# Kernel tuning notes

Measured on AMD Instinct MI355X. Metric: run time of the kernel, lower is better.

Reference implementation:

```python
import jax, jax.numpy as jnp
import numpy as np

B, T, HID = 16, 512, 1024
NH, NKV, D = 8, 4, 128
THETA = 10000.0


def setup_inputs() -> dict:
    key = jax.random.key(0)
    k0, k1, k2, k3, k4 = jax.random.split(key, 5)
    s = 0.02
    return {
        "hidden_states": jax.random.normal(k0, (B, T, HID), dtype=jnp.float32),
        "Wq": s * jax.random.normal(k1, (HID, NH * D), dtype=jnp.float32),
        "Wk": s * jax.random.normal(k2, (HID, NKV * D), dtype=jnp.float32),
        "Wv": s * jax.random.normal(k3, (HID, NKV * D), dtype=jnp.float32),
        "Wo": s * jax.random.normal(k4, (NH * D, HID), dtype=jnp.float32),
    }


def _rotate_half(x):
    x1, x2 = x[..., : x.shape[-1] // 2], x[..., x.shape[-1] // 2:]
    return jnp.concatenate((-x2, x1), axis=-1)


def reference(hidden_states, Wq, Wk, Wv, Wo):
    b, t, _ = hidden_states.shape
    # projections -> [B, H, T, D]
    q = (hidden_states @ Wq).reshape(b, t, NH, D).transpose(0, 2, 1, 3)
    k = (hidden_states @ Wk).reshape(b, t, NKV, D).transpose(0, 2, 1, 3)
    v = (hidden_states @ Wv).reshape(b, t, NKV, D).transpose(0, 2, 1, 3)

    # RoPE: cos/sin [T, D]
    inv_freq = 1.0 / (THETA ** (jnp.arange(0, D, 2, dtype=jnp.float32) / D))
    freqs = jnp.outer(jnp.arange(t, dtype=jnp.float32), inv_freq)
    emb = jnp.concatenate((freqs, freqs), axis=-1)
    cos, sin = jnp.cos(emb), jnp.sin(emb)
    q = q * cos + _rotate_half(q) * sin
    k = k * cos + _rotate_half(k) * sin

    # repeat_interleave KV heads to match query heads (GQA)
    groups = NH // NKV
    k = jnp.repeat(k, groups, axis=1)  # [B, NH, T, D]
    v = jnp.repeat(v, groups, axis=1)

    scale = 1.0 / jnp.sqrt(jnp.float32(D))
    attn = jnp.einsum("bhtd,bhsd->bhts", q, k) * scale  # [B, NH, T, T]
    causal = jnp.triu(jnp.ones((t, t), dtype=bool), k=1)
    attn = jnp.where(causal, -jnp.inf, attn)
    attn = jax.nn.softmax(attn, axis=-1)  # dropout p=0 (eval)

    out = jnp.einsum("bhts,bhsd->bhtd", attn, v)
    out = out.transpose(0, 2, 1, 3).reshape(b, t, NH * D)
    return out @ Wo  # [B, T, HID]
```

## Files before the change

### kernel.cpp

```cpp
#include <hip/hip_runtime.h>
#include <hip/hip_bf16.h>
#include <math.h>

#define Bn 16
#define Tn 512
#define HIDn 1024
#define NHn 8
#define NKVn 4
#define Dn 128

typedef __attribute__((ext_vector_type(8))) short short8;
typedef __attribute__((ext_vector_type(4))) float floatx4;

__device__ __forceinline__ short bf16r(float f) {
  __hip_bfloat16 h = __float2bfloat16(f);
  return *(short*)&h;
}
__device__ __forceinline__ float bf16f(short s) {
  __hip_bfloat16 h = *(__hip_bfloat16*)&s;
  return __bfloat162float(h);
}

__device__ __forceinline__ void g2l16(const short* g, short* l) {
  __builtin_amdgcn_global_load_lds(
      (const __attribute__((address_space(1))) void*)g,
      (__attribute__((address_space(3))) void*)l, 16, 0, 0);
}

__global__ __launch_bounds__(256) void prep_kernel(const float* __restrict__ X,
                                                   const float* __restrict__ Wq,
                                                   const float* __restrict__ Wk,
                                                   const float* __restrict__ Wv,
                                                   const float* __restrict__ Wo,
                                                   short* __restrict__ Xb,
                                                   short* __restrict__ BtQKV,
                                                   short* __restrict__ Wot) {
  __shared__ float tile[32][33];
  int bid = blockIdx.x;
  if (bid < 4096) {
    int i = bid * 256 + threadIdx.x;
    const float4* p = reinterpret_cast<const float4*>(X) + (size_t)i * 2;
    float4 a = p[0], b = p[1];
    short8 o;
    o[0] = bf16r(a.x); o[1] = bf16r(a.y); o[2] = bf16r(a.z); o[3] = bf16r(a.w);
    o[4] = bf16r(b.x); o[5] = bf16r(b.y); o[6] = bf16r(b.z); o[7] = bf16r(b.w);
    reinterpret_cast<short8*>(Xb)[i] = o;
    return;
  }
  int t = bid - 4096;
  const float* in;
  short* out;
  int N;
  if (t < 1024)      { in = Wq; out = BtQKV;               N = 1024; }
  else if (t < 1536) { t -= 1024; in = Wk; out = BtQKV + 1024 * 1024; N = 512; }
  else if (t < 2048) { t -= 1536; in = Wv; out = BtQKV + 1536 * 1024; N = 512; }
  else               { t -= 2048; in = Wo; out = Wot;                N = 1024; }
  int ntx = N >> 5;
  int n0 = (t % ntx) * 32, k0 = (t / ntx) * 32;
  int tx = threadIdx.x & 31, ty = threadIdx.x >> 5;
  for (int i = 0; i < 32; i += 8)
    tile[ty + i][tx] = in[(size_t)(k0 + ty + i) * N + n0 + tx];
  __syncthreads();
  for (int i = 0; i < 32; i += 8)
    out[(size_t)(n0 + ty + i) * 1024 + k0 + tx] = bf16r(tile[tx][ty + i]);
}

__global__ __launch_bounds__(256) void gemm_qkv(const short* __restrict__ A,
                                                const short* __restrict__ Bt,
                                                short* __restrict__ Cqkv,
                                                short* __restrict__ Vt) {
  __shared__ __align__(16) short SH[128 * 136];
  short* As = SH;
  short* Bs = SH + 128 * 64;
  const int K = 1024, N = 2048;
  const int tid = threadIdx.x;
  const int wave = tid >> 6, lane = tid & 63;
  const int quad = lane >> 4, l16 = lane & 15;
  const int wrow = wave >> 1, wcol = wave & 1;
  const int m0 = blockIdx.y * 128, n0 = blockIdx.x * 128;
  floatx4 acc[4][4];
  for (int mi = 0; mi < 4; ++mi)
    for (int ni = 0; ni < 4; ++ni)
      acc[mi][ni] = (floatx4){0.f, 0.f, 0.f, 0.f};

  for (int kt = 0; kt < K; kt += 64) {
#pragma unroll
    for (int v = 0; v < 4; ++v) {
      int s = tid + v * 256;
      int r = s >> 3;
      int c = (s & 7) ^ (r & 7);
      short* dstA = As + (size_t)(v * 256 + wave * 64) * 8;
      g2l16(&A[(size_t)(m0 + r) * K + kt + c * 8], dstA);
      short* dstB = Bs + (size_t)(v * 256 + wave * 64) * 8;
      g2l16(&Bt[(size_t)(n0 + r) * K + kt + c * 8], dstB);
    }
    __syncthreads();
#pragma unroll
    for (int kc = 0; kc < 2; ++kc) {
      short8 af[4], bfr[4];
#pragma unroll
      for (int mi = 0; mi < 4; ++mi) {
        int R = wrow * 64 + mi * 16 + l16;
        int pos = (kc * 4 + quad) ^ (R & 7);
        af[mi] = *(short8*)&As[R * 64 + pos * 8];
      }
#pragma unroll
      for (int ni = 0; ni < 4; ++ni) {
        int R = wcol * 64 + ni * 16 + l16;
        int pos = (kc * 4 + quad) ^ (R & 7);
        bfr[ni] = *(short8*)&Bs[R * 64 + pos * 8];
      }
#pragma unroll
      for (int mi = 0; mi < 4; ++mi)
#pragma unroll
        for (int ni = 0; ni < 4; ++ni)
          acc[mi][ni] = __builtin_amdgcn_mfma_f32_16x16x32_bf16(af[mi], bfr[ni], acc[mi][ni], 0, 0, 0);
    }
    __syncthreads();
  }

  const int bx = blockIdx.x;
  if (bx < 12) {
#pragma unroll
    for (int mi = 0; mi < 4; ++mi)
#pragma unroll
      for (int ni = 0; ni < 4; ++ni)
#pragma unroll
        for (int r = 0; r < 4; ++r) {
          int row = m0 + wrow * 64 + mi * 16 + quad * 4 + r;
          int col = n0 + wcol * 64 + ni * 16 + l16;
          Cqkv[(size_t)row * N + col] = bf16r(acc[mi][ni][r]);
        }
  } else {
#pragma unroll
    for (int mi = 0; mi < 4; ++mi)
#pragma unroll
      for (int ni = 0; ni < 4; ++ni)
#pragma unroll
        for (int r = 0; r < 4; ++r) {
          int tl = wrow * 64 + mi * 16 + quad * 4 + r;
          int dl = wcol * 64 + ni * 16 + l16;
          SH[dl * 136 + tl] = bf16r(acc[mi][ni][r]);
        }
    __syncthreads();
    int kv = bx - 12, b = m0 >> 9, t0 = m0 & (Tn - 1);
#pragma unroll
    for (int k2 = 0; k2 < 8; ++k2) {
      int c = k2 * 256 + tid;
      int d = c >> 4, toff = (c & 15) << 3;
      short8 v = *(short8*)&SH[d * 136 + toff];
      *(short8*)&Vt[((size_t)(b * NKVn + kv) * 128 + d) * Tn + t0 + toff] = v;
    }
  }
}

__global__ void rope_k_kernel(short* __restrict__ C) {
  int idx = blockIdx.x * blockDim.x + threadIdx.x;
  int vec = idx & 7;
  int head = (idx >> 3) & 3;
  int bt = idx >> 5;
  int t = bt & (Tn - 1);
  int i0 = vec * 8;
  size_t base = (size_t)bt * 2048 + 1024 + head * 128 + i0;
  short8 x1 = *(short8*)&C[base];
  short8 x2 = *(short8*)&C[base + 64];
  short8 o1, o2;
  float tf = (float)t;
#pragma unroll
  for (int j = 0; j < 8; ++j) {
    float a = tf * exp2f(-0.2076205059f * (float)(i0 + j));
    float s, c;
    sincosf(a, &s, &c);
    float v1 = bf16f(x1[j]), v2 = bf16f(x2[j]);
    o1[j] = bf16r(v1 * c - v2 * s);
    o2[j] = bf16r(v2 * c + v1 * s);
  }
  *(short8*)&C[base] = o1;
  *(short8*)&C[base + 64] = o2;
}

template <bool OUTF32>
__global__ __launch_bounds__(256) void gemm_bt(const short* __restrict__ A,
                                               const short* __restrict__ Bt,
                                               void* __restrict__ Cout,
                                               int M, int N, int K) {
  __shared__ __align__(16) short As[128 * 64];
  __shared__ __align__(16) short Bs[128 * 64];
  const int tid = threadIdx.x;
  const int wave = tid >> 6, lane = tid & 63;
  const int quad = lane >> 4, l16 = lane & 15;
  const int wrow = wave >> 1, wcol = wave & 1;
  const int m0 = blockIdx.y * 128, n0 = blockIdx.x * 128;
  floatx4 acc[4][4];
  for (int mi = 0; mi < 4; ++mi)
    for (int ni = 0; ni < 4; ++ni)
      acc[mi][ni] = (floatx4){0.f, 0.f, 0.f, 0.f};

  for (int kt = 0; kt < K; kt += 64) {
#pragma unroll
    for (int v = 0; v < 4; ++v) {
      int s = tid + v * 256;
      int r = s >> 3;
      int c = (s & 7) ^ (r & 7);
      short* dstA = (short*)As + (size_t)(v * 256 + wave * 64) * 8;
      g2l16(&A[(size_t)(m0 + r) * K + kt + c * 8], dstA);
      short* dstB = (short*)Bs + (size_t)(v * 256 + wave * 64) * 8;
      g2l16(&Bt[(size_t)(n0 + r) * K + kt + c * 8], dstB);
    }
    __syncthreads();
#pragma unroll
    for (int kc = 0; kc < 2; ++kc) {
      short8 af[4], bfr[4];
#pragma unroll
      for (int mi = 0; mi < 4; ++mi) {
        int R = wrow * 64 + mi * 16 + l16;
        int pos = (kc * 4 + quad) ^ (R & 7);
        af[mi] = *(short8*)&As[R * 64 + pos * 8];
      }
#pragma unroll
      for (int ni = 0; ni < 4; ++ni) {
        int R = wcol * 64 + ni * 16 + l16;
        int pos = (kc * 4 + quad) ^ (R & 7);
        bfr[ni] = *(short8*)&Bs[R * 64 + pos * 8];
      }
#pragma unroll
      for (int mi = 0; mi < 4; ++mi)
#pragma unroll
        for (int ni = 0; ni < 4; ++ni)
          acc[mi][ni] = __builtin_amdgcn_mfma_f32_16x16x32_bf16(af[mi], bfr[ni], acc[mi][ni], 0, 0, 0);
    }
    __syncthreads();
  }
#pragma unroll
  for (int mi = 0; mi < 4; ++mi)
#pragma unroll
    for (int ni = 0; ni < 4; ++ni)
#pragma unroll
      for (int r = 0; r < 4; ++r) {
        int row = m0 + wrow * 64 + mi * 16 + quad * 4 + r;
        int col = n0 + wcol * 64 + ni * 16 + l16;
        if (OUTF32)
          ((float*)Cout)[(size_t)row * N + col] = acc[mi][ni][r];
        else
          ((short*)Cout)[(size_t)row * N + col] = bf16r(acc[mi][ni][r]);
      }
}

__global__ __launch_bounds__(256) void attn_kernel(const short* __restrict__ Cqkv,
                                                   const short* __restrict__ Vt,
                                                   short* __restrict__ Aout) {
  __shared__ __align__(16) short Ks[64 * 128];
  __shared__ __align__(16) short Vs[128 * 64];
  __shared__ short Ps[4][16][72];
  const int tid = threadIdx.x;
  const int wave = tid >> 6, lane = tid & 63;
  const int quad = lane >> 4, l16 = lane & 15;
  const int blk = blockIdx.x;
  const int qt = 7 - (blk >> 7);
  const int h = blk & 7, b = (blk >> 3) & 15;
  const int kvh = h >> 1;
  const short* Qp = Cqkv + (size_t)b * Tn * 2048 + h * 128;
  const short* Kp = Cqkv + (size_t)b * Tn * 2048 + 1024 + kvh * 128;
  const short* Vtp = Vt + (size_t)(b * NKVn + kvh) * 128 * Tn;

  const int qrow0 = qt * 64 + wave * 16;
  const float scale = 0.08838834764831845f;

  short8 qf[4];
#pragma unroll
  for (int kc = 0; kc < 4; ++kc)
    qf[kc] = *(const short8*)&Qp[(size_t)(qrow0 + l16) * 2048 + kc * 32 + quad * 8];
  {
    float tf = (float)(qrow0 + l16);
#pragma unroll
    for (int kc = 0; kc < 2; ++kc)
#pragma unroll
      for (int j = 0; j < 8; ++j) {
        int d = kc * 32 + quad * 8 + j;
        float a = tf * exp2f(-0.2076205059f * (float)d);
        float s, c;
        sincosf(a, &s, &c);
        float x1 = bf16f(qf[kc][j]), x2 = bf16f(qf[kc + 2][j]);
        qf[kc][j] = bf16r((x1 * c - x2 * s) * scale);
        qf[kc + 2][j] = bf16r((x2 * c + x1 * s) * scale);
      }
  }

  floatx4 o[8];
  float l_part[4];
#pragma unroll
  for (int ni = 0; ni < 8; ++ni) o[ni] = (floatx4){0.f, 0.f, 0.f, 0.f};
#pragma unroll
  for (int r = 0; r < 4; ++r) l_part[r] = 0.f;

  const int nk = qt * 64 + 64;

  for (int k0 = 0; k0 < nk; k0 += 64) {
#pragma unroll
    for (int v = 0; v < 4; ++v) {
      int s = tid + v * 256;
      int r = s >> 4, c = (s & 15) ^ (r & 15);
      short* dstK = (short*)Ks + (size_t)(v * 256 + wave * 64) * 8;
      g2l16(&Kp[(size_t)(k0 + r) * 2048 + c * 8], dstK);
    }
#pragma unroll
    for (int v = 0; v < 4; ++v) {
      int s = tid + v * 256;
      int r = s >> 3, c = (s & 7) ^ (r & 7);
      short* dstV = (short*)Vs + (size_t)(v * 256 + wave * 64) * 8;
      g2l16(&Vtp[(size_t)r * Tn + k0 + c * 8], dstV);
    }
    __syncthreads();

    floatx4 s[4];
#pragma unroll
    for (int ni = 0; ni < 4; ++ni) {
      s[ni] = (floatx4){0.f, 0.f, 0.f, 0.f};
      short8 kf[4];
#pragma unroll
      for (int kc = 0; kc < 4; ++kc) {
        int R = ni * 16 + l16;
        int pos = (kc * 4 + quad) ^ (R & 15);
        kf[kc] = *(short8*)&Ks[R * 128 + pos * 8];
      }
#pragma unroll
      for (int kc = 0; kc < 4; ++kc)
        s[ni] = __builtin_amdgcn_mfma_f32_16x16x32_bf16(qf[kc], kf[kc], s[ni], 0, 0, 0);
    }

    const bool diag = (k0 + 63 > qrow0);
#pragma unroll
    for (int ni = 0; ni < 4; ++ni)
#pragma unroll
      for (int r = 0; r < 4; ++r) {
        float p = __expf(s[ni][r]);
        if (diag) {
          int key = k0 + ni * 16 + l16;
          int qr = qrow0 + quad * 4 + r;
          if (key > qr) p = 0.f;
        }
        s[ni][r] = p;
        l_part[r] += p;
      }

#pragma unroll
    for (int ni = 0; ni < 4; ++ni)
#pragma unroll
      for (int r = 0; r < 4; ++r)
        Ps[wave][quad * 4 + r][ni * 16 + l16] = bf16r(s[ni][r]);

    short8 pf[2];
#pragma unroll
    for (int kc = 0; kc < 2; ++kc)
      pf[kc] = *(short8*)&Ps[wave][l16][kc * 32 + quad * 8];
#pragma unroll
    for (int ni = 0; ni < 8; ++ni) {
      int R = ni * 16 + l16;
      int pos0 = quad ^ (R & 7);
      int pos1 = (4 + quad) ^ (R & 7);
      short8 vf0 = *(short8*)&Vs[R * 64 + pos0 * 8];
      short8 vf1 = *(short8*)&Vs[R * 64 + pos1 * 8];
      o[ni] = __builtin_amdgcn_mfma_f32_16x16x32_bf16(pf[0], vf0, o[ni], 0, 0, 0);
      o[ni] = __builtin_amdgcn_mfma_f32_16x16x32_bf16(pf[1], vf1, o[ni], 0, 0, 0);
    }
    __syncthreads();
  }

  float inv[4];
#pragma unroll
  for (int r = 0; r < 4; ++r) {
    float rs = l_part[r];
#pragma unroll
    for (int off = 8; off >= 1; off >>= 1) rs += __shfl_xor(rs, off, 16);
    inv[r] = 1.0f / rs;
  }
#pragma unroll
  for (int ni = 0; ni < 8; ++ni)
#pragma unroll
    for (int r = 0; r < 4; ++r) {
      int t = qrow0 + quad * 4 + r;
      int d = ni * 16 + l16;
      Aout[((size_t)b * Tn + t) * 1024 + h * 128 + d] = bf16r(o[ni][r] * inv[r]);
    }
}

extern "C" void kernel_launch(void* const* d_in, const int* in_sizes, int n_in,
                              void* d_out, int out_size, void* d_ws, size_t ws_size,
                              hipStream_t stream) {
  const float* X  = (const float*)d_in[0];
  const float* Wq = (const float*)d_in[1];
  const float* Wk = (const float*)d_in[2];
  const float* Wv = (const float*)d_in[3];
  const float* Wo = (const float*)d_in[4];

  char* ws = (char*)d_ws;
  short* Xb    = (short*)(ws);
  short* BtQKV = (short*)(ws + (16ull << 20));
  short* Wot   = (short*)(ws + (20ull << 20));
  short* Cqkv  = (short*)(ws + (22ull << 20));
  short* Vt    = (short*)(ws + (54ull << 20));
  short* Aout  = (short*)(ws + (62ull << 20));

  prep_kernel<<<7168, 256, 0, stream>>>(X, Wq, Wk, Wv, Wo, Xb, BtQKV, Wot);
  gemm_qkv<<<dim3(16, 64), 256, 0, stream>>>(Xb, BtQKV, Cqkv, Vt);
  rope_k_kernel<<<1024, 256, 0, stream>>>(Cqkv);
  attn_kernel<<<1024, 256, 0, stream>>>(Cqkv, Vt, Aout);
  gemm_bt<true><<<dim3(8, 64), 256, 0, stream>>>(Aout, Wot, d_out, 8192, 1024, 1024);
}
```

Baseline: 196.4 us.

## Rewrite QKV GEMM as 256x256 tile, 8-wave, double-buffered pipelined kernel

The QKV projection GEMM moves from a 128x128 tile with 4 waves and single-buffered LDS to a 256x256 tile with 8 waves, double-buffered LDS and global-to-LDS loads issued ahead by two k-steps. The work is split into four quadrant phases that interleave async loads with MFMA bursts, using raised wave priority and explicit vmcnt waits. A block-index swizzle is added for L2 locality. The V-transpose epilogue is adapted to the larger tile, processing two KV heads per block. The goal is to hide memory latency and raise arithmetic intensity per LDS byte. The costs are fewer blocks (256), heavier register pressure under launch_bounds(512,2), and 128KB of LDS per block.

```diff
diff --git a/kernel.cpp b/kernel.cpp
--- a/kernel.cpp
+++ b/kernel.cpp
@@ -65,93 +65,182 @@
     out[(size_t)(n0 + ty + i) * 1024 + k0 + tx] = bf16r(tile[tx][ty + i]);
 }
 
-__global__ __launch_bounds__(256) void gemm_qkv(const short* __restrict__ A,
-                                                const short* __restrict__ Bt,
-                                                short* __restrict__ Cqkv,
-                                                short* __restrict__ Vt) {
-  __shared__ __align__(16) short SH[128 * 136];
-  short* As = SH;
-  short* Bs = SH + 128 * 64;
-  const int K = 1024, N = 2048;
+__global__ __launch_bounds__(512, 2) void gemm_qkv(const short* __restrict__ A,
+                                                   const short* __restrict__ Bt,
+                                                   short* __restrict__ Cqkv,
+                                                   short* __restrict__ Vt) {
+  __shared__ __align__(16) short SH[65536];
   const int tid = threadIdx.x;
   const int wave = tid >> 6, lane = tid & 63;
   const int quad = lane >> 4, l16 = lane & 15;
-  const int wrow = wave >> 1, wcol = wave & 1;
-  const int m0 = blockIdx.y * 128, n0 = blockIdx.x * 128;
-  floatx4 acc[4][4];
-  for (int mi = 0; mi < 4; ++mi)
-    for (int ni = 0; ni < 4; ++ni)
-      acc[mi][ni] = (floatx4){0.f, 0.f, 0.f, 0.f};
-
-  for (int kt = 0; kt < K; kt += 64) {
-#pragma unroll
-    for (int v = 0; v < 4; ++v) {
-      int s = tid + v * 256;
-      int r = s >> 3;
-      int c = (s & 7) ^ (r & 7);
-      short* dstA = As + (size_t)(v * 256 + wave * 64) * 8;
-      g2l16(&A[(size_t)(m0 + r) * K + kt + c * 8], dstA);
-      short* dstB = Bs + (size_t)(v * 256 + wave * 64) * 8;
-      g2l16(&Bt[(size_t)(n0 + r) * K + kt + c * 8], dstB);
-    }
-    __syncthreads();
-#pragma unroll
-    for (int kc = 0; kc < 2; ++kc) {
-      short8 af[4], bfr[4];
-#pragma unroll
-      for (int mi = 0; mi < 4; ++mi) {
-        int R = wrow * 64 + mi * 16 + l16;
-        int pos = (kc * 4 + quad) ^ (R & 7);
-        af[mi] = *(short8*)&As[R * 64 + pos * 8];
-      }
-#pragma unroll
-      for (int ni = 0; ni < 4; ++ni) {
-        int R = wcol * 64 + ni * 16 + l16;
-        int pos = (kc * 4 + quad) ^ (R & 7);
-        bfr[ni] = *(short8*)&Bs[R * 64 + pos * 8];
-      }
+  const int wr = wave >> 2, wc = wave & 3;
+  int fid = blockIdx.y * 8 + blockIdx.x;
+  int swz = (fid & 7) * 32 + (fid >> 3);
+  const int bx = swz & 7;
+  const int m0 = (swz >> 3) << 8, n0 = bx << 8;
+  const int nt = 16;
+
+  floatx4 acc[2][2][4][2];
+#pragma unroll
+  for (int r = 0; r < 2; ++r)
+#pragma unroll
+    for (int c = 0; c < 2; ++c)
 #pragma unroll
       for (int mi = 0; mi < 4; ++mi)
 #pragma unroll
-        for (int ni = 0; ni < 4; ++ni)
-          acc[mi][ni] = __builtin_amdgcn_mfma_f32_16x16x32_bf16(af[mi], bfr[ni], acc[mi][ni], 0, 0, 0);
-    }
-    __syncthreads();
-  }
-
-  const int bx = blockIdx.x;
-  if (bx < 12) {
-#pragma unroll
-    for (int mi = 0; mi < 4; ++mi)
-#pragma unroll
-      for (int ni = 0; ni < 4; ++ni)
-#pragma unroll
-        for (int r = 0; r < 4; ++r) {
-          int row = m0 + wrow * 64 + mi * 16 + quad * 4 + r;
-          int col = n0 + wcol * 64 + ni * 16 + l16;
-          Cqkv[(size_t)row * N + col] = bf16r(acc[mi][ni][r]);
-        }
+        for (int ni = 0; ni < 2; ++ni)
+          acc[r][c][mi][ni] = (floatx4){0.f, 0.f, 0.f, 0.f};
+
+  const int srow = tid >> 3;
+  const int schunk = (tid & 7) ^ (srow & 7);
+
+#define STAGE(tile_, src_, row0_, ldso_)                                             \
+  do {                                                                               \
+    int t_ = (tile_);                                                                \
+    if (t_ < nt) {                                                                   \
+      short* bb_ = SH + ((t_ & 1) << 15) + (ldso_);                                  \
+      const short* sp_ =                                                             \
+          (src_) + ((size_t)((row0_) + srow) << 10) + (t_ << 6) + (schunk << 3);     \
+      g2l16(sp_, bb_ + (wave << 9));                                                 \
+      g2l16(sp_ + (64 << 10), bb_ + 4096 + (wave << 9));                             \
+    }                                                                                \
+  } while (0)
+
+#define LDA(rhalf_)                                                                  \
+  do {                                                                               \
+    _Pragma("unroll") for (int mi = 0; mi < 4; ++mi) {                               \
+      int R = (rhalf_) * 128 + wr * 64 + mi * 16 + l16;                              \
+      _Pragma("unroll") for (int k = 0; k < 2; ++k) {                                \
+        int pos = (k * 4 + quad) ^ (R & 7);                                          \
+        af[mi][k] = *(const short8*)&Ab[R * 64 + pos * 8];                           \
+      }                                                                              \
+    }                                                                                \
+  } while (0)
+
+#define LDB(dst_, chalf_)                                                            \
+  do {                                                                               \
+    _Pragma("unroll") for (int ni = 0; ni < 2; ++ni) {                               \
+      int R = (chalf_) * 128 + wc * 32 + ni * 16 + l16;                              \
+      _Pragma("unroll") for (int k = 0; k < 2; ++k) {                                \
+        int pos = (k * 4 + quad) ^ (R & 7);                                          \
+        dst_[ni][k] = *(const short8*)&Bb[R * 64 + pos * 8];                         \
+      }                                                                              \
+    }                                                                                \
+  } while (0)
+
+#define MFMA_Q(r_, c_, bf_)                                                          \
+  do {                                                                               \
+    _Pragma("unroll") for (int mi = 0; mi < 4; ++mi)                                 \
+        _Pragma("unroll") for (int ni = 0; ni < 2; ++ni) {                           \
+      acc[r_][c_][mi][ni] = __builtin_amdgcn_mfma_f32_16x16x32_bf16(                 \
+          af[mi][0], bf_[ni][0], acc[r_][c_][mi][ni], 0, 0, 0);                      \
+      acc[r_][c_][mi][ni] = __builtin_amdgcn_mfma_f32_16x16x32_bf16(                 \
+          af[mi][1], bf_[ni][1], acc[r_][c_][mi][ni], 0, 0, 0);                      \
+    }                                                                                \
+  } while (0)
+
+#define PH_OPEN()                                                                    \
+  do {                                                                               \
+    __builtin_amdgcn_s_barrier();                                                    \
+    asm volatile("s_waitcnt lgkmcnt(0)");                                            \
+    __builtin_amdgcn_s_setprio(1);                                                   \
+  } while (0)
+#define PH_CLOSE()                                                                   \
+  do {                                                                               \
+    __builtin_amdgcn_s_setprio(0);                                                   \
+    __builtin_amdgcn_s_barrier();                                                    \
+  } while (0)
+
+  STAGE(0, A, m0, 0);
+  STAGE(0, Bt, n0 + 128, 24576);
+  STAGE(0, Bt, n0, 16384);
+  STAGE(0, A, m0 + 128, 8192);
+  STAGE(1, A, m0, 0);
+  STAGE(1, Bt, n0 + 128, 24576);
+  STAGE(1, Bt, n0, 16384);
+  asm volatile("s_waitcnt vmcnt(6)" ::: "memory");
+  __builtin_amdgcn_s_barrier();
+
+  short8 af[4][2], bf0[2][2], bf1[2][2];
+  for (int g = 0; g < nt; ++g) {
+    const short* Ab = SH + ((g & 1) << 15);
+    const short* Bb = Ab + 16384;
+    LDA(0);
+    LDB(bf0, 0);
+    STAGE(g + 1, A, m0 + 128, 8192);
+    PH_OPEN();
+    MFMA_Q(0, 0, bf0);
+    PH_CLOSE();
+    LDB(bf1, 1);
+    STAGE(g + 2, A, m0, 0);
+    PH_OPEN();
+    MFMA_Q(0, 1, bf1);
+    PH_CLOSE();
+    LDA(1);
+    STAGE(g + 2, Bt, n0 + 128, 24576);
+    PH_OPEN();
+    MFMA_Q(1, 1, bf1);
+    PH_CLOSE();
+    STAGE(g + 2, Bt, n0, 16384);
+    PH_OPEN();
+    MFMA_Q(1, 0, bf0);
+    __builtin_amdgcn_s_setprio(0);
+    if (g + 2 < nt)
+      asm volatile("s_waitcnt vmcnt(6)" ::: "memory");
+    else
+      asm volatile("s_waitcnt vmcnt(0)" ::: "memory");
+    __builtin_amdgcn_s_barrier();
+  }
+
+  if (bx < 6) {
+#pragma unroll
+    for (int r = 0; r < 2; ++r)
+#pragma unroll
+      for (int c = 0; c < 2; ++c)
+#pragma unroll
+        for (int mi = 0; mi < 4; ++mi)
+#pragma unroll
+          for (int ni = 0; ni < 2; ++ni)
+#pragma unroll
+            for (int rr = 0; rr < 4; ++rr) {
+              int row = m0 + r * 128 + wr * 64 + mi * 16 + quad * 4 + rr;
+              int col = n0 + c * 128 + wc * 32 + ni * 16 + l16;
+              Cqkv[(size_t)row * 2048 + col] = bf16r(acc[r][c][mi][ni][rr]);
+            }
   } else {
-#pragma unroll
-    for (int mi = 0; mi < 4; ++mi)
-#pragma unroll
-      for (int ni = 0; ni < 4; ++ni)
-#pragma unroll
-        for (int r = 0; r < 4; ++r) {
-          int tl = wrow * 64 + mi * 16 + quad * 4 + r;
-          int dl = wcol * 64 + ni * 16 + l16;
-          SH[dl * 136 + tl] = bf16r(acc[mi][ni][r]);
-        }
-    __syncthreads();
-    int kv = bx - 12, b = m0 >> 9, t0 = m0 & (Tn - 1);
-#pragma unroll
-    for (int k2 = 0; k2 < 8; ++k2) {
-      int c = k2 * 256 + tid;
-      int d = c >> 4, toff = (c & 15) << 3;
-      short8 v = *(short8*)&SH[d * 136 + toff];
-      *(short8*)&Vt[((size_t)(b * NKVn + kv) * 128 + d) * Tn + t0 + toff] = v;
-    }
-  }
+    const int b = m0 >> 9, t0 = m0 & (Tn - 1);
+#pragma unroll
+    for (int ch = 0; ch < 2; ++ch) {
+      __syncthreads();
+#pragma unroll
+      for (int r = 0; r < 2; ++r)
+#pragma unroll
+        for (int mi = 0; mi < 4; ++mi)
+#pragma unroll
+          for (int ni = 0; ni < 2; ++ni)
+#pragma unroll
+            for (int rr = 0; rr < 4; ++rr) {
+              int t = r * 128 + wr * 64 + mi * 16 + quad * 4 + rr;
+              int d = wc * 32 + ni * 16 + l16;
+              SH[d * 264 + t] = bf16r(acc[r][ch][mi][ni][rr]);
+            }
+      __syncthreads();
+      int kv = (bx - 6) * 2 + ch;
+#pragma unroll
+      for (int u = 0; u < 8; ++u) {
+        int idx = tid + u * 512;
+        int d = idx >> 5, tb = (idx & 31) << 3;
+        short8 vv = *(short8*)&SH[d * 264 + tb];
+        *(short8*)&Vt[((size_t)(b * NKVn + kv) * 128 + d) * Tn + t0 + tb] = vv;
+      }
+    }
+  }
+#undef STAGE
+#undef LDA
+#undef LDB
+#undef MFMA_Q
+#undef PH_OPEN
+#undef PH_CLOSE
 }
 
 __global__ void rope_k_kernel(short* __restrict__ C) {
@@ -402,7 +491,7 @@
   short* Aout  = (short*)(ws + (62ull << 20));
 
   prep_kernel<<<7168, 256, 0, stream>>>(X, Wq, Wk, Wv, Wo, Xb, BtQKV, Wot);
-  gemm_qkv<<<dim3(16, 64), 256, 0, stream>>>(Xb, BtQKV, Cqkv, Vt);
+  gemm_qkv<<<dim3(8, 32), 512, 0, stream>>>(Xb, BtQKV, Cqkv, Vt);
   rope_k_kernel<<<1024, 256, 0, stream>>>(Cqkv);
   attn_kernel<<<1024, 256, 0, stream>>>(Cqkv, Vt, Aout);
   gemm_bt<true><<<dim3(8, 64), 256, 0, stream>>>(Aout, Wot, d_out, 8192, 1024, 1024);
```

New measurement: 182.1 us. 7.3% less time.
